# Optimization experiments

Hardware: AMD Instinct MI355X
Metric: run time of the kernel (lower is better)

Reference implementation:

```python
import jax, jax.numpy as jnp
import numpy as np

B, C, H, W = 4, 512, 64, 64
CQK = C // 8  # query/key channels


def setup_inputs() -> dict:
    key = jax.random.key(0)
    ks = jax.random.split(key, 8)
    s = 0.05
    return {
        "x": jax.random.normal(ks[0], (B, C, H, W), dtype=jnp.float32),
        "Wq": jax.random.normal(ks[1], (CQK, C), dtype=jnp.float32) * s,
        "bq": jax.random.normal(ks[2], (CQK,), dtype=jnp.float32) * s,
        "Wk": jax.random.normal(ks[3], (CQK, C), dtype=jnp.float32) * s,
        "bk": jax.random.normal(ks[4], (CQK,), dtype=jnp.float32) * s,
        "Wv": jax.random.normal(ks[5], (C, C), dtype=jnp.float32) * s,
        "bv": jax.random.normal(ks[6], (C,), dtype=jnp.float32) * s,
        "gamma": jax.random.normal(ks[7], (1,), dtype=jnp.float32),
    }


def reference(x, Wq, bq, Wk, bk, Wv, bv, gamma):
    b, c, h, w = x.shape
    hw = h * w
    # 1x1 convs == per-pixel linear projections over channels
    q = jnp.einsum('bchw,dc->bdhw', x, Wq) + bq[None, :, None, None]
    k = jnp.einsum('bchw,dc->bdhw', x, Wk) + bk[None, :, None, None]
    v = jnp.einsum('bchw,dc->bdhw', x, Wv) + bv[None, :, None, None]
    q = q.reshape(b, -1, hw)  # [B, C/8, HW]
    k = k.reshape(b, -1, hw)  # [B, C/8, HW]
    v = v.reshape(b, -1, hw)  # [B, C,   HW]
    # attn[b,i,j] = <q[:, i], k[:, j]>, softmax over j
    attn = jax.nn.softmax(jnp.einsum('bdi,bdj->bij', q, k), axis=-1)
    # out[b,c,i] = sum_j v[b,c,j] * attn[b,i,j]
    out = jnp.einsum('bcj,bij->bci', v, attn).reshape(b, c, h, w)
    return gamma[0] * out + x
```

## Files before the change

kernel.cpp:

```cpp
#include <hip/hip_runtime.h>
#include <hip/hip_bf16.h>
#include <math.h>

#define HW 4096
#define NC 512
#define NB 4

typedef float f32x4 __attribute__((ext_vector_type(4)));
typedef float f32x16 __attribute__((ext_vector_type(16)));
typedef short bf16x8 __attribute__((ext_vector_type(8)));
typedef unsigned int u32;
typedef u32 u32x4 __attribute__((ext_vector_type(4)));
typedef unsigned short ushort_t;

#define GLOAD_LDS(g, s) __builtin_amdgcn_global_load_lds((const __attribute__((address_space(1))) void*)(g), (__attribute__((address_space(3))) void*)(s), 16, 0, 0)

__device__ __forceinline__ unsigned short f2bf(float f){
  unsigned int u = __builtin_bit_cast(unsigned int, f);
  u += 0x7FFFu + ((u >> 16) & 1u);
  return (unsigned short)(u >> 16);
}
__device__ __forceinline__ float bf2f(unsigned short h){
  unsigned int u = ((unsigned int)h) << 16;
  return __builtin_bit_cast(float, u);
}

__global__ __launch_bounds__(256) void wsplit_kernel(
    const float* __restrict__ Wq, const float* __restrict__ Wk,
    const float* __restrict__ Wv, ushort_t* __restrict__ wh, ushort_t* __restrict__ wl)
{
  long e = ((long)blockIdx.x * 256 + threadIdx.x) * 8;
  int r = (int)(e >> 9), c = (int)(e & 511);
  const float* src = (r < 64)  ? Wq + (long)r * 512 + c
                   : (r < 128) ? Wk + (long)(r - 64) * 512 + c
                               : Wv + (long)(r - 128) * 512 + c;
  f32x4 v0 = *reinterpret_cast<const f32x4*>(src);
  f32x4 v1 = *reinterpret_cast<const f32x4*>(src + 4);
  ushort_t h[8], l[8];
  #pragma unroll
  for (int j = 0; j < 4; j++){ h[j] = f2bf(v0[j]); l[j] = f2bf(v0[j] - bf2f(h[j])); }
  #pragma unroll
  for (int j = 0; j < 4; j++){ h[4+j] = f2bf(v1[j]); l[4+j] = f2bf(v1[j] - bf2f(h[4+j])); }
  *reinterpret_cast<bf16x8*>(wh + e) = *reinterpret_cast<bf16x8*>(h);
  if (r < 128) *reinterpret_cast<bf16x8*>(wl + e) = *reinterpret_cast<bf16x8*>(l);
}

__global__ __launch_bounds__(256) void split_kernel(
    const float* __restrict__ x, ushort_t* __restrict__ xth, ushort_t* __restrict__ xtl)
{
  const int i0 = blockIdx.x * 64;
  const int c0 = blockIdx.y * 64;
  const int b  = blockIdx.z;
  const int tid = threadIdx.x;
  const int tx = tid & 63, ty = tid >> 6;
  __shared__ float ts[64][65];
  #pragma unroll
  for (int u = 0; u < 16; u++){
    int cl = ty * 16 + u;
    ts[cl][tx] = x[((long)b * NC + c0 + cl) * HW + i0 + tx];
  }
  __syncthreads();
  const int px = tid >> 2;
  const int cs = (tid & 3) * 16;
  ushort_t h[16], l[16];
  #pragma unroll
  for (int e = 0; e < 16; e++){
    float v = ts[cs + e][px];
    h[e] = f2bf(v);
    l[e] = f2bf(v - bf2f(h[e]));
  }
  long base = ((long)b * HW + i0 + px) * 512 + c0 + cs;
  *reinterpret_cast<bf16x8*>(xth + base)     = *reinterpret_cast<bf16x8*>(h);
  *reinterpret_cast<bf16x8*>(xth + base + 8) = *reinterpret_cast<bf16x8*>(h + 8);
  *reinterpret_cast<bf16x8*>(xtl + base)     = *reinterpret_cast<bf16x8*>(l);
  *reinterpret_cast<bf16x8*>(xtl + base + 8) = *reinterpret_cast<bf16x8*>(l + 8);
}

__global__ __launch_bounds__(256) void gemm_kernel(
    const ushort_t* __restrict__ xth, const ushort_t* __restrict__ xtl,
    const ushort_t* __restrict__ wh, const ushort_t* __restrict__ wl,
    const float* __restrict__ bq, const float* __restrict__ bk, const float* __restrict__ bv,
    ushort_t* __restrict__ qhi, ushort_t* __restrict__ qlo,
    ushort_t* __restrict__ khi, ushort_t* __restrict__ klo,
    ushort_t* __restrict__ vv)
{
  extern __shared__ char lds[];
  const int it = blockIdx.x;
  const int rg = blockIdx.y;
  const int b  = blockIdx.z;
  const int i0 = it * 128;
  const int tid = threadIdx.x;
  const int w = tid >> 6;
  const int lane = tid & 63;
  const int g = lane >> 4, n = lane & 15;
  const int wy = w >> 1, wx = w & 1;

  f32x4 acc[4][4];
  #pragma unroll
  for (int a = 0; a < 4; a++)
    #pragma unroll
    for (int m = 0; m < 4; m++) acc[a][m] = (f32x4){0.f, 0.f, 0.f, 0.f};

  const long xrow = (long)b * HW + i0;

  auto stage = [&](int bsel, int c0s){
    char* dbase = lds + bsel * 32768 + (w << 10);
    #pragma unroll
    for (int u = 0; u < 4; u++){
      int idx = (u << 8) | tid;
      int px = idx >> 3;
      int chs = (idx & 7) ^ (px & 7);
      long go = (xrow + px) * 512 + c0s + chs * 8;
      GLOAD_LDS(xth + go, dbase + (u << 12));
      GLOAD_LDS(xtl + go, dbase + 16384 + (u << 12));
    }
  };

  stage(0, 0);
  asm volatile("s_waitcnt vmcnt(0)" ::: "memory");
  __syncthreads();

  int cur = 0;
  for (int t = 0; t < 8; t++){
    const int c0 = t << 6;
    bf16x8 wfh[4][2], wfl[4][2];
    #pragma unroll
    for (int a = 0; a < 4; a++){
      long R = (long)(rg * 128 + wx * 64 + a * 16 + n) * 512 + c0 + g * 8;
      wfh[a][0] = *reinterpret_cast<const bf16x8*>(wh + R);
      wfh[a][1] = *reinterpret_cast<const bf16x8*>(wh + R + 32);
    }
    if (rg == 0){
      #pragma unroll
      for (int a = 0; a < 4; a++){
        long R = (long)(wx * 64 + a * 16 + n) * 512 + c0 + g * 8;
        wfl[a][0] = *reinterpret_cast<const bf16x8*>(wl + R);
        wfl[a][1] = *reinterpret_cast<const bf16x8*>(wl + R + 32);
      }
    }
    if (t < 7) stage(cur ^ 1, (t + 1) << 6);
    bf16x8 xh[4][2], xl[4][2];
    const char* buf = lds + cur * 32768;
    #pragma unroll
    for (int m = 0; m < 4; m++){
      int px = wy * 64 + m * 16 + n;
      const char* row = buf + px * 128;
      #pragma unroll
      for (int ks = 0; ks < 2; ks++){
        int off = (((ks << 2) | g) ^ (px & 7)) << 4;
        xh[m][ks] = *reinterpret_cast<const bf16x8*>(row + off);
        xl[m][ks] = *reinterpret_cast<const bf16x8*>(row + 16384 + off);
      }
    }
    __builtin_amdgcn_s_setprio(1);
    if (rg == 0){
      #pragma unroll
      for (int a = 0; a < 4; a++)
        #pragma unroll
        for (int m = 0; m < 4; m++)
          #pragma unroll
          for (int ks = 0; ks < 2; ks++){
            acc[a][m] = __builtin_amdgcn_mfma_f32_16x16x32_bf16(xh[m][ks], wfh[a][ks], acc[a][m], 0, 0, 0);
            acc[a][m] = __builtin_amdgcn_mfma_f32_16x16x32_bf16(xl[m][ks], wfh[a][ks], acc[a][m], 0, 0, 0);
            acc[a][m] = __builtin_amdgcn_mfma_f32_16x16x32_bf16(xh[m][ks], wfl[a][ks], acc[a][m], 0, 0, 0);
          }
    } else {
      #pragma unroll
      for (int a = 0; a < 4; a++)
        #pragma unroll
        for (int m = 0; m < 4; m++)
          #pragma unroll
          for (int ks = 0; ks < 2; ks++){
            acc[a][m] = __builtin_amdgcn_mfma_f32_16x16x32_bf16(wfh[a][ks], xh[m][ks], acc[a][m], 0, 0, 0);
            acc[a][m] = __builtin_amdgcn_mfma_f32_16x16x32_bf16(wfh[a][ks], xl[m][ks], acc[a][m], 0, 0, 0);
          }
    }
    __builtin_amdgcn_s_setprio(0);
    asm volatile("s_waitcnt vmcnt(0)" ::: "memory");
    __syncthreads();
    cur ^= 1;
  }

  if (rg == 0){
    ushort_t* hs = wx ? khi : qhi;
    ushort_t* ls = wx ? klo : qlo;
    const float* bias = wx ? bk : bq;
    const float qscale = wx ? 1.0f : 1.44269504088896f;
    #pragma unroll
    for (int a = 0; a < 4; a++){
      float bb = bias[a * 16 + n];
      #pragma unroll
      for (int m = 0; m < 4; m++){
        #pragma unroll
        for (int r4 = 0; r4 < 4; r4++){
          int px = wy * 64 + m * 16 + g * 4 + r4;
          float v = (acc[a][m][r4] + bb) * qscale;
          ushort_t h = f2bf(v);
          ushort_t l = f2bf(v - bf2f(h));
          long ad = (xrow + px) * 64 + a * 16 + n;
          hs[ad] = h;
          ls[ad] = l;
        }
      }
    }
  } else {
    #pragma unroll
    for (int a = 0; a < 4; a++){
      #pragma unroll
      for (int r4 = 0; r4 < 4; r4++){
        int C = (rg - 1) * 128 + wx * 64 + a * 16 + g * 4 + r4;
        float bb = bv[C];
        #pragma unroll
        for (int m = 0; m < 4; m++){
          int px = wy * 64 + m * 16 + n;
          vv[((long)b * NC + C) * HW + i0 + px] = f2bf(acc[a][m][r4] + bb);
        }
      }
    }
  }
}

__global__ __launch_bounds__(512, 1) void attn_kernel(
    const ushort_t* __restrict__ qhi, const ushort_t* __restrict__ qlo,
    const ushort_t* __restrict__ khi,
    const ushort_t* __restrict__ vv,
    ushort_t* __restrict__ p0, ushort_t* __restrict__ p1,
    float* __restrict__ mbuf, float* __restrict__ lbuf)
{
  extern __shared__ char smem[];
  const int wgid = blockIdx.x;
  const int xcd = wgid & 7;
  const int jh = xcd >> 2;
  const int b  = xcd & 3;
  const int qt = wgid >> 3;
  const int tid = threadIdx.x;
  const int w = tid >> 6;
  const int lane = tid & 63;
  const int q32 = lane & 31;
  const int hh = lane >> 5;
  const int rg = w >> 1, ch = w & 1;
  const int i0w = qt * 128 + rg * 32;
  const int c0w = ch * 256;
  const int jbase = jh * 2048;

  const int kj = tid >> 3;
  const int kdblk = (tid & 7) ^ (kj & 7);
  const long kgbase = ((long)b * HW + kj) * 64 + kdblk * 8;

  auto stageK = [&](int bsel, int j0){
    char* dst = smem + bsel * 8192 + (tid >> 6 << 10);
    GLOAD_LDS(khi + kgbase + (long)j0 * 64, dst);
  };
  auto stageV = [&](int bsel, int j0){
    char* dbase = smem + 16384 + bsel * 65536 + (w << 10);
    #pragma unroll
    for (int r = 0; r < 8; r++){
      int ss = (r << 9) | tid;
      int c = ss >> 3;
      int jblk = (ss & 7) ^ (c & 7);
      long goff = (long)b * (NC * HW) + (long)c * HW + j0 + jblk * 8;
      GLOAD_LDS(vv + goff, dbase + (r << 13));
    }
  };

  bf16x8 aqh[4], aql[4];
  #pragma unroll
  for (int c = 0; c < 4; c++){
    long qb = ((long)b * HW + i0w + q32) * 64 + c * 16 + hh * 8;
    aqh[c] = *reinterpret_cast<const bf16x8*>(qhi + qb);
    aql[c] = *reinterpret_cast<const bf16x8*>(qlo + qb);
  }

  f32x16 acc[8];
  #pragma unroll
  for (int ct = 0; ct < 8; ct++)
    #pragma unroll
    for (int r = 0; r < 16; r++) acc[ct][r] = 0.f;
  float mrow = -1e30f, lrow = 0.f;

  stageK(0, jbase);
  stageV(0, jbase);
  asm volatile("s_waitcnt vmcnt(0)" ::: "memory");
  __syncthreads();

  int cur = 0;
  for (int t = 0; t < 32; t++){
    if (t < 31){
      stageK(cur ^ 1, jbase + (t + 1) * 64);
      stageV(cur ^ 1, jbase + (t + 1) * 64);
    }
    f32x16 sv[2];
    {
      const char* kb0 = smem + cur * 8192;
      __builtin_amdgcn_s_setprio(1);
      #pragma unroll
      for (int jt = 0; jt < 2; jt++){
        int jrow = jt * 32 + q32;
        const char* krow = kb0 + jrow * 128;
        int r7 = jrow & 7;
        f32x16 s;
        #pragma unroll
        for (int r = 0; r < 16; r++) s[r] = 0.f;
        #pragma unroll
        for (int c = 0; c < 4; c++){
          int off = (((c << 1) | hh) ^ r7) << 4;
          bf16x8 kh = *(const bf16x8*)(krow + off);
          s = __builtin_amdgcn_mfma_f32_32x32x16_bf16(kh, aqh[c], s, 0, 0, 0);
          s = __builtin_amdgcn_mfma_f32_32x32x16_bf16(kh, aql[c], s, 0, 0, 0);
        }
        sv[jt] = s;
      }
      __builtin_amdgcn_s_setprio(0);
    }
    {
      f32x16 mx;
      #pragma unroll
      for (int r = 0; r < 16; r++) mx[r] = fmaxf(sv[0][r], sv[1][r]);
      float m8[8];
      #pragma unroll
      for (int r = 0; r < 8; r++) m8[r] = fmaxf(mx[r], mx[r + 8]);
      float m4a = fmaxf(m8[0], m8[4]), m4b = fmaxf(m8[1], m8[5]);
      float m4c = fmaxf(m8[2], m8[6]), m4d = fmaxf(m8[3], m8[7]);
      float tmx = fmaxf(fmaxf(m4a, m4b), fmaxf(m4c, m4d));
      tmx = fmaxf(tmx, __shfl_xor(tmx, 32));
      if (__any(tmx > mrow + 11.5f)){
        float mnew = fmaxf(mrow, tmx);
        float sc = exp2f(mrow - mnew);
        lrow *= sc;
        #pragma unroll
        for (int ct = 0; ct < 8; ct++)
          #pragma unroll
          for (int r = 0; r < 16; r++) acc[ct][r] *= sc;
        mrow = mnew;
      }
    }
    bf16x8 pa[4];
    {
      #pragma unroll
      for (int jt = 0; jt < 2; jt++)
        #pragma unroll
        for (int r = 0; r < 16; r++) sv[jt][r] = exp2f(sv[jt][r] - mrow);
      float rs = 0.f;
      #pragma unroll
      for (int r = 0; r < 16; r++) rs += sv[0][r] + sv[1][r];
      rs += __shfl_xor(rs, 32);
      lrow += rs;
      #pragma unroll
      for (int jt = 0; jt < 2; jt++){
        u32 pk[8];
        #pragma unroll
        for (int i = 0; i < 8; i++){
          float a = sv[jt][2 * i], bb = sv[jt][2 * i + 1];
          u32 d;
          asm("v_cvt_pk_bf16_f32 %0, %1, %2" : "=v"(d) : "v"(a), "v"(bb));
          pk[i] = d;
        }
        #pragma unroll
        for (int cc = 0; cc < 2; cc++){
          u32 a0 = pk[4 * cc + 0], b0 = pk[4 * cc + 2];
          u32 a1 = pk[4 * cc + 1], b1 = pk[4 * cc + 3];
          asm volatile("v_permlane32_swap_b32 %0, %1" : "+v"(a0), "+v"(b0));
          asm volatile("v_permlane32_swap_b32 %0, %1" : "+v"(a1), "+v"(b1));
          u32x4 wv;
          wv[0] = a0; wv[1] = a1; wv[2] = b0; wv[3] = b1;
          pa[jt * 2 + cc] = __builtin_bit_cast(bf16x8, wv);
        }
      }
    }
    {
      const char* vb = smem + 16384 + cur * 65536;
      __builtin_amdgcn_s_setprio(1);
      #pragma unroll
      for (int ct = 0; ct < 8; ct++){
        int row = c0w + ct * 32 + q32;
        const char* vrow = vb + row * 128;
        int r7 = row & 7;
        #pragma unroll
        for (int c = 0; c < 4; c++){
          int off = (((c << 1) | hh) ^ r7) << 4;
          bf16x8 vf = *(const bf16x8*)(vrow + off);
          acc[ct] = __builtin_amdgcn_mfma_f32_32x32x16_bf16(vf, pa[c], acc[ct], 0, 0, 0);
        }
      }
      __builtin_amdgcn_s_setprio(0);
    }
    asm volatile("s_waitcnt vmcnt(0)" ::: "memory");
    __syncthreads();
    cur ^= 1;
  }

  ushort_t* pd = jh ? p1 : p0;
  const int i = i0w + q32;
  #pragma unroll
  for (int ct = 0; ct < 8; ct++){
    #pragma unroll
    for (int r = 0; r < 16; r++){
      int c = c0w + ct * 32 + (r & 3) + 8 * (r >> 2) + 4 * hh;
      pd[((long)b * NC + c) * HW + i] = f2bf(acc[ct][r]);
    }
  }
  if (ch == 0 && lane < 32){
    int gi = b * HW + i0w + lane;
    mbuf[jh * (NB * HW) + gi] = mrow;
    lbuf[jh * (NB * HW) + gi] = lrow;
  }
}

__global__ __launch_bounds__(256) void comb_kernel(
    const ushort_t* __restrict__ p0, const ushort_t* __restrict__ p1,
    const float* __restrict__ mbuf, const float* __restrict__ lbuf,
    const float* __restrict__ x, const float* __restrict__ gamma,
    float* __restrict__ out)
{
  const int it = blockIdx.x;
  const int ct = blockIdx.y;
  const int b  = blockIdx.z;
  const int i0 = it * 64, c0 = ct * 64;
  const int tid = threadIdx.x;
  const int tx = tid & 63, ty = tid >> 6;
  __shared__ float f0s[64], f1s[64];
  const float gm = gamma[0];
  if (tid < 64){
    int gi = b * HW + i0 + tid;
    float m0 = mbuf[gi], m1 = mbuf[NB * HW + gi];
    float l0 = lbuf[gi], l1 = lbuf[NB * HW + gi];
    float M = fmaxf(m0, m1);
    float w0 = exp2f(m0 - M), w1 = exp2f(m1 - M);
    float rden = 1.f / (w0 * l0 + w1 * l1);
    f0s[tid] = w0 * rden;
    f1s[tid] = w1 * rden;
  }
  __syncthreads();
  #pragma unroll
  for (int u = 0; u < 16; u++){
    int cl = ty * 16 + u;
    long idx = ((long)b * NC + c0 + cl) * HW + i0 + tx;
    float o = f0s[tx] * bf2f(p0[idx]) + f1s[tx] * bf2f(p1[idx]);
    out[idx] = fmaf(gm, o, x[idx]);
  }
}

extern "C" void kernel_launch(void* const* d_in, const int* in_sizes, int n_in,
                              void* d_out, int out_size, void* d_ws, size_t ws_size,
                              hipStream_t stream)
{
  const float* x  = (const float*)d_in[0];
  const float* Wq = (const float*)d_in[1];
  const float* bq = (const float*)d_in[2];
  const float* Wk = (const float*)d_in[3];
  const float* bk = (const float*)d_in[4];
  const float* Wv = (const float*)d_in[5];
  const float* bv = (const float*)d_in[6];
  const float* gamma = (const float*)d_in[7];
  float* out = (float*)d_out;

  char* ws = (char*)d_ws;
  const size_t MB = 1024 * 1024;
  ushort_t* xth = (ushort_t*)(ws);
  ushort_t* xtl = (ushort_t*)(ws + 16 * MB);
  ushort_t* wh  = (ushort_t*)(ws + 32 * MB);
  ushort_t* wl  = (ushort_t*)(ws + 32 * MB + 655360);
  ushort_t* qhi = (ushort_t*)(ws + 33 * MB);
  ushort_t* qlo = (ushort_t*)(ws + 35 * MB);
  ushort_t* khi = (ushort_t*)(ws + 37 * MB);
  ushort_t* klo = (ushort_t*)(ws + 39 * MB);
  ushort_t* vv  = (ushort_t*)(ws + 41 * MB);
  float*    mbuf = (float*)(ws + 57 * MB);
  float*    lbuf = (float*)(ws + 57 * MB + 131072);
  ushort_t* part0 = xth;
  ushort_t* part1 = xtl;

  wsplit_kernel<<<dim3(160), dim3(256), 0, stream>>>(Wq, Wk, Wv, wh, wl);
  split_kernel<<<dim3(64, 8, NB), dim3(256), 0, stream>>>(x, xth, xtl);

  const int GSMEM = 65536;
  hipFuncSetAttribute((const void*)gemm_kernel,
                      hipFuncAttributeMaxDynamicSharedMemorySize, GSMEM);
  gemm_kernel<<<dim3(32, 5, NB), dim3(256), GSMEM, stream>>>(
      xth, xtl, wh, wl, bq, bk, bv, qhi, qlo, khi, klo, vv);

  const int ASMEM = 147456;
  hipFuncSetAttribute((const void*)attn_kernel,
                      hipFuncAttributeMaxDynamicSharedMemorySize, ASMEM);
  attn_kernel<<<dim3(256), dim3(512), ASMEM, stream>>>(
      qhi, qlo, khi, vv, part0, part1, mbuf, lbuf);

  comb_kernel<<<dim3(64, 8, NB), dim3(256), 0, stream>>>(
      part0, part1, mbuf, lbuf, x, gamma, out);
}
```

Measured before the change: 212.0 us.

## Split attention waves into producers that compute softmax and consumers that load

Before, the two waves sharing a 32-row group each recomputed the same QK scores and softmax. Now four producer waves compute S and P once and pass P, plus the per-row rescale flag and factor, to their paired consumer waves through LDS. The consumer waves issue all global-to-LDS loads for the next V and K tiles. K drops to a single buffer, LDS use grows, and an extra block barrier is added each iteration. The split leaves the producers with more work than the consumers (QK, softmax and their own PV share), which may leave the consumers idle at the barrier.

Result: faster. 198.2 us (-6.5%).

```diff
diff --git a/kernel.cpp b/kernel.cpp
--- a/kernel.cpp
+++ b/kernel.cpp
@@ -228,6 +228,7 @@
     float* __restrict__ mbuf, float* __restrict__ lbuf)
 {
   extern __shared__ char smem[];
+  const int VB = 8192, PB = 139264, FB = 155648;
   const int wgid = blockIdx.x;
   const int xcd = wgid & 7;
   const int jh = xcd >> 2;
@@ -238,65 +239,55 @@
   const int lane = tid & 63;
   const int q32 = lane & 31;
   const int hh = lane >> 5;
-  const int rg = w >> 1, ch = w & 1;
+  const bool producer = (w < 4);
+  const int rg = producer ? w : (w - 4);
+  const int ch = producer ? 0 : 1;
   const int i0w = qt * 128 + rg * 32;
   const int c0w = ch * 256;
   const int jbase = jh * 2048;
-
-  const int kj = tid >> 3;
-  const int kdblk = (tid & 7) ^ (kj & 7);
-  const long kgbase = ((long)b * HW + kj) * 64 + kdblk * 8;
-
-  auto stageK = [&](int bsel, int j0){
-    char* dst = smem + bsel * 8192 + (tid >> 6 << 10);
-    GLOAD_LDS(khi + kgbase + (long)j0 * 64, dst);
-  };
-  auto stageV = [&](int bsel, int j0){
-    char* dbase = smem + 16384 + bsel * 65536 + (w << 10);
+  const int ct256 = ((w & 3) << 6) | lane;
+
+  bf16x8 aqh[4], aql[4];
+  #pragma unroll
+  for (int c = 0; c < 4; c++){
+    long qb = ((long)b * HW + i0w + q32) * 64 + c * 16 + hh * 8;
+    aqh[c] = *reinterpret_cast<const bf16x8*>(qhi + qb);
+    aql[c] = *reinterpret_cast<const bf16x8*>(qlo + qb);
+  }
+
+  f32x16 acc[8];
+  #pragma unroll
+  for (int ct = 0; ct < 8; ct++)
+    #pragma unroll
+    for (int r = 0; r < 16; r++) acc[ct][r] = 0.f;
+  float mrow = -1e30f, lrow = 0.f;
+
+  {
+    int kj = tid >> 3;
+    int kd = (tid & 7) ^ (kj & 7);
+    GLOAD_LDS(khi + ((long)b * HW + jbase + kj) * 64 + kd * 8, smem + (w << 10));
     #pragma unroll
     for (int r = 0; r < 8; r++){
       int ss = (r << 9) | tid;
       int c = ss >> 3;
       int jblk = (ss & 7) ^ (c & 7);
-      long goff = (long)b * (NC * HW) + (long)c * HW + j0 + jblk * 8;
-      GLOAD_LDS(vv + goff, dbase + (r << 13));
-    }
-  };
-
-  bf16x8 aqh[4], aql[4];
-  #pragma unroll
-  for (int c = 0; c < 4; c++){
-    long qb = ((long)b * HW + i0w + q32) * 64 + c * 16 + hh * 8;
-    aqh[c] = *reinterpret_cast<const bf16x8*>(qhi + qb);
-    aql[c] = *reinterpret_cast<const bf16x8*>(qlo + qb);
-  }
-
-  f32x16 acc[8];
-  #pragma unroll
-  for (int ct = 0; ct < 8; ct++)
-    #pragma unroll
-    for (int r = 0; r < 16; r++) acc[ct][r] = 0.f;
-  float mrow = -1e30f, lrow = 0.f;
-
-  stageK(0, jbase);
-  stageV(0, jbase);
+      GLOAD_LDS(vv + ((long)b * NC + c) * HW + jbase + jblk * 8,
+                smem + VB + (r << 13) + (w << 10));
+    }
+  }
   asm volatile("s_waitcnt vmcnt(0)" ::: "memory");
   __syncthreads();
 
   int cur = 0;
   for (int t = 0; t < 32; t++){
-    if (t < 31){
-      stageK(cur ^ 1, jbase + (t + 1) * 64);
-      stageV(cur ^ 1, jbase + (t + 1) * 64);
-    }
-    f32x16 sv[2];
-    {
-      const char* kb0 = smem + cur * 8192;
+    bf16x8 pa[4];
+    if (producer){
+      f32x16 sv[2];
       __builtin_amdgcn_s_setprio(1);
       #pragma unroll
       for (int jt = 0; jt < 2; jt++){
         int jrow = jt * 32 + q32;
-        const char* krow = kb0 + jrow * 128;
+        const char* krow = smem + jrow * 128;
         int r7 = jrow & 7;
         f32x16 s;
         #pragma unroll
@@ -311,8 +302,6 @@
         sv[jt] = s;
       }
       __builtin_amdgcn_s_setprio(0);
-    }
-    {
       f32x16 mx;
       #pragma unroll
       for (int r = 0; r < 16; r++) mx[r] = fmaxf(sv[0][r], sv[1][r]);
@@ -323,9 +312,11 @@
       float m4c = fmaxf(m8[2], m8[6]), m4d = fmaxf(m8[3], m8[7]);
       float tmx = fmaxf(fmaxf(m4a, m4b), fmaxf(m4c, m4d));
       tmx = fmaxf(tmx, __shfl_xor(tmx, 32));
-      if (__any(tmx > mrow + 11.5f)){
+      int upd = __any(tmx > mrow + 11.5f) ? 1 : 0;
+      float sc = 1.f;
+      if (upd){
         float mnew = fmaxf(mrow, tmx);
-        float sc = exp2f(mrow - mnew);
+        sc = exp2f(mrow - mnew);
         lrow *= sc;
         #pragma unroll
         for (int ct = 0; ct < 8; ct++)
@@ -333,9 +324,6 @@
           for (int r = 0; r < 16; r++) acc[ct][r] *= sc;
         mrow = mnew;
       }
-    }
-    bf16x8 pa[4];
-    {
       #pragma unroll
       for (int jt = 0; jt < 2; jt++)
         #pragma unroll
@@ -366,9 +354,53 @@
           pa[jt * 2 + cc] = __builtin_bit_cast(bf16x8, wv);
         }
       }
+      char* pb = smem + PB + rg * 4096 + lane * 64;
+      #pragma unroll
+      for (int i = 0; i < 4; i++)
+        *reinterpret_cast<bf16x8*>(pb + ((i ^ (lane & 3)) << 4)) = pa[i];
+      if (lane == 0) *(int*)(smem + FB + rg * 4) = upd;
+      if (upd && hh == 0) *(float*)(smem + FB + 64 + rg * 128 + q32 * 4) = sc;
+    } else {
+      if (t < 31){
+        char* dbase = smem + VB + ((cur ^ 1) << 16) + ((w & 3) << 10);
+        int j0 = jbase + (t + 1) * 64;
+        #pragma unroll
+        for (int r = 0; r < 16; r++){
+          int ss = (r << 8) | ct256;
+          int c = ss >> 3;
+          int jblk = (ss & 7) ^ (c & 7);
+          GLOAD_LDS(vv + ((long)b * NC + c) * HW + j0 + jblk * 8, dbase + (r << 12));
+        }
+      }
+    }
+    __syncthreads();
+    if (!producer){
+      if (t < 31){
+        int j0 = jbase + (t + 1) * 64;
+        #pragma unroll
+        for (int r = 0; r < 2; r++){
+          int chunk = (r << 8) | ct256;
+          int kj = chunk >> 3;
+          int kd = (chunk & 7) ^ (kj & 7);
+          GLOAD_LDS(khi + ((long)b * HW + j0 + kj) * 64 + kd * 8,
+                    smem + (r << 12) + ((w & 3) << 10));
+        }
+      }
+      const char* pb = smem + PB + rg * 4096 + lane * 64;
+      #pragma unroll
+      for (int i = 0; i < 4; i++)
+        pa[i] = *reinterpret_cast<const bf16x8*>(pb + ((i ^ (lane & 3)) << 4));
+      int updf = *(const int*)(smem + FB + rg * 4);
+      if (updf){
+        float sc = *(const float*)(smem + FB + 64 + rg * 128 + q32 * 4);
+        #pragma unroll
+        for (int ct = 0; ct < 8; ct++)
+          #pragma unroll
+          for (int r = 0; r < 16; r++) acc[ct][r] *= sc;
+      }
     }
     {
-      const char* vb = smem + 16384 + cur * 65536;
+      const char* vb = smem + VB + (cur << 16);
       __builtin_amdgcn_s_setprio(1);
       #pragma unroll
       for (int ct = 0; ct < 8; ct++){
@@ -399,7 +431,7 @@
       pd[((long)b * NC + c) * HW + i] = f2bf(acc[ct][r]);
     }
   }
-  if (ch == 0 && lane < 32){
+  if (producer && lane < 32){
     int gi = b * HW + i0w + lane;
     mbuf[jh * (NB * HW) + gi] = mrow;
     lbuf[jh * (NB * HW) + gi] = lrow;
@@ -479,7 +511,7 @@
   gemm_kernel<<<dim3(32, 5, NB), dim3(256), GSMEM, stream>>>(
       xth, xtl, wh, wl, bq, bk, bv, qhi, qlo, khi, klo, vv);
 
-  const int ASMEM = 147456;
+  const int ASMEM = 156672;
   hipFuncSetAttribute((const void*)attn_kernel,
                       hipFuncAttributeMaxDynamicSharedMemorySize, ASMEM);
   attn_kernel<<<dim3(256), dim3(512), ASMEM, stream>>>(
```

## Software-pipeline attention loop with 32-key tiles and triple-buffered V

Applied to the files above, without the earlier changes.

Restructures the attention main loop to work on 32-key tiles instead of 64. V is triple-buffered and K double-buffered, with loads issued two tiles ahead, and the QK^T plus softmax for the next tile is computed after the current PV MFMAs. This lets softmax overlap with outstanding loads and MFMA work. The wait now drains only partially (vmcnt(4)) before the barrier instead of fully, and LDS use drops. In exchange there are twice as many barriers and iterations, and the hi/lo QK products go into separate accumulators that are summed afterwards.

After: 218.8 us. 3.2% more time.

```diff
diff --git a/kernel.cpp b/kernel.cpp
--- a/kernel.cpp
+++ b/kernel.cpp
@@ -228,6 +228,7 @@
     float* __restrict__ mbuf, float* __restrict__ lbuf)
 {
   extern __shared__ char smem[];
+  const int KB = 98304;
   const int wgid = blockIdx.x;
   const int xcd = wgid & 7;
   const int jh = xcd >> 2;
@@ -243,26 +244,6 @@
   const int c0w = ch * 256;
   const int jbase = jh * 2048;
 
-  const int kj = tid >> 3;
-  const int kdblk = (tid & 7) ^ (kj & 7);
-  const long kgbase = ((long)b * HW + kj) * 64 + kdblk * 8;
-
-  auto stageK = [&](int bsel, int j0){
-    char* dst = smem + bsel * 8192 + (tid >> 6 << 10);
-    GLOAD_LDS(khi + kgbase + (long)j0 * 64, dst);
-  };
-  auto stageV = [&](int bsel, int j0){
-    char* dbase = smem + 16384 + bsel * 65536 + (w << 10);
-    #pragma unroll
-    for (int r = 0; r < 8; r++){
-      int ss = (r << 9) | tid;
-      int c = ss >> 3;
-      int jblk = (ss & 7) ^ (c & 7);
-      long goff = (long)b * (NC * HW) + (long)c * HW + j0 + jblk * 8;
-      GLOAD_LDS(vv + goff, dbase + (r << 13));
-    }
-  };
-
   bf16x8 aqh[4], aql[4];
   #pragma unroll
   for (int c = 0; c < 4; c++){
@@ -277,116 +258,140 @@
     #pragma unroll
     for (int r = 0; r < 16; r++) acc[ct][r] = 0.f;
   float mrow = -1e30f, lrow = 0.f;
+  bf16x8 pa[2];
+
+  auto stageV = [&](int vbsel, int j0){
+    char* vd = smem + vbsel * 32768;
+    #pragma unroll
+    for (int u = 0; u < 4; u++){
+      int ci = (w << 8) | (u << 6) | lane;
+      int R = ci >> 3, half = (ci >> 2) & 1, pos = ci & 3;
+      int jc = pos ^ (R & 3);
+      int c = 2 * R + half;
+      GLOAD_LDS(vv + ((long)b * NC + c) * HW + j0 + jc * 8, vd + ci * 16);
+    }
+  };
+  auto stageK = [&](int kbsel, int j0){
+    if (lane < 32){
+      int ci = (w << 5) | lane;
+      int kj = ci >> 3, pos = ci & 7;
+      int db = pos ^ (kj & 7);
+      GLOAD_LDS(khi + ((long)b * HW + j0 + kj) * 64 + db * 8,
+                smem + KB + (kbsel << 12) + ci * 16);
+    }
+  };
+
+  auto qk_sm = [&](int tt){
+    const char* krow = smem + KB + ((tt & 1) << 12) + q32 * 128;
+    const int r7 = q32 & 7;
+    f32x16 s1, s2;
+    #pragma unroll
+    for (int r = 0; r < 16; r++){ s1[r] = 0.f; s2[r] = 0.f; }
+    __builtin_amdgcn_s_setprio(1);
+    #pragma unroll
+    for (int c = 0; c < 4; c++){
+      int off = (((c << 1) | hh) ^ r7) << 4;
+      bf16x8 kh = *(const bf16x8*)(krow + off);
+      s1 = __builtin_amdgcn_mfma_f32_32x32x16_bf16(kh, aqh[c], s1, 0, 0, 0);
+      s2 = __builtin_amdgcn_mfma_f32_32x32x16_bf16(kh, aql[c], s2, 0, 0, 0);
+    }
+    __builtin_amdgcn_s_setprio(0);
+    f32x16 sv;
+    #pragma unroll
+    for (int r = 0; r < 16; r++) sv[r] = s1[r] + s2[r];
+    float m8[8];
+    #pragma unroll
+    for (int r = 0; r < 8; r++) m8[r] = fmaxf(sv[r], sv[r + 8]);
+    float m4a = fmaxf(m8[0], m8[4]), m4b = fmaxf(m8[1], m8[5]);
+    float m4c = fmaxf(m8[2], m8[6]), m4d = fmaxf(m8[3], m8[7]);
+    float tmx = fmaxf(fmaxf(m4a, m4b), fmaxf(m4c, m4d));
+    tmx = fmaxf(tmx, __shfl_xor(tmx, 32));
+    if (__any(tmx > mrow + 11.5f)){
+      float mnew = fmaxf(mrow, tmx);
+      float sc = exp2f(mrow - mnew);
+      lrow *= sc;
+      #pragma unroll
+      for (int ct = 0; ct < 8; ct++)
+        #pragma unroll
+        for (int r = 0; r < 16; r++) acc[ct][r] *= sc;
+      mrow = mnew;
+    }
+    #pragma unroll
+    for (int r = 0; r < 16; r++) sv[r] = exp2f(sv[r] - mrow);
+    float rs = 0.f;
+    #pragma unroll
+    for (int r = 0; r < 16; r++) rs += sv[r];
+    rs += __shfl_xor(rs, 32);
+    lrow += rs;
+    u32 pk[8];
+    #pragma unroll
+    for (int i = 0; i < 8; i++){
+      float a = sv[2 * i], bb = sv[2 * i + 1];
+      u32 d;
+      asm("v_cvt_pk_bf16_f32 %0, %1, %2" : "=v"(d) : "v"(a), "v"(bb));
+      pk[i] = d;
+    }
+    #pragma unroll
+    for (int cc = 0; cc < 2; cc++){
+      u32 a0 = pk[4 * cc + 0], b0 = pk[4 * cc + 2];
+      u32 a1 = pk[4 * cc + 1], b1 = pk[4 * cc + 3];
+      asm volatile("v_permlane32_swap_b32 %0, %1" : "+v"(a0), "+v"(b0));
+      asm volatile("v_permlane32_swap_b32 %0, %1" : "+v"(a1), "+v"(b1));
+      u32x4 wv;
+      wv[0] = a0; wv[1] = a1; wv[2] = b0; wv[3] = b1;
+      pa[cc] = __builtin_bit_cast(bf16x8, wv);
+    }
+  };
 
   stageK(0, jbase);
+  stageK(1, jbase + 32);
   stageV(0, jbase);
+  stageV(1, jbase + 32);
   asm volatile("s_waitcnt vmcnt(0)" ::: "memory");
-  __syncthreads();
-
-  int cur = 0;
-  for (int t = 0; t < 32; t++){
-    if (t < 31){
-      stageK(cur ^ 1, jbase + (t + 1) * 64);
-      stageV(cur ^ 1, jbase + (t + 1) * 64);
-    }
-    f32x16 sv[2];
+  __builtin_amdgcn_s_barrier();
+  __builtin_amdgcn_sched_barrier(0);
+
+  qk_sm(0);
+  __builtin_amdgcn_sched_barrier(0);
+  __builtin_amdgcn_s_barrier();
+  __builtin_amdgcn_sched_barrier(0);
+
+  for (int t = 0; t < 64; t++){
+    if (t < 62){
+      int j2 = jbase + (t + 2) * 32;
+      stageK(t & 1, j2);
+      stageV((t + 2) % 3, j2);
+    }
     {
-      const char* kb0 = smem + cur * 8192;
+      const char* vb = smem + (t % 3) * 32768;
       __builtin_amdgcn_s_setprio(1);
       #pragma unroll
-      for (int jt = 0; jt < 2; jt++){
-        int jrow = jt * 32 + q32;
-        const char* krow = kb0 + jrow * 128;
-        int r7 = jrow & 7;
-        f32x16 s;
-        #pragma unroll
-        for (int r = 0; r < 16; r++) s[r] = 0.f;
-        #pragma unroll
-        for (int c = 0; c < 4; c++){
-          int off = (((c << 1) | hh) ^ r7) << 4;
-          bf16x8 kh = *(const bf16x8*)(krow + off);
-          s = __builtin_amdgcn_mfma_f32_32x32x16_bf16(kh, aqh[c], s, 0, 0, 0);
-          s = __builtin_amdgcn_mfma_f32_32x32x16_bf16(kh, aql[c], s, 0, 0, 0);
-        }
-        sv[jt] = s;
-      }
-      __builtin_amdgcn_s_setprio(0);
-    }
-    {
-      f32x16 mx;
-      #pragma unroll
-      for (int r = 0; r < 16; r++) mx[r] = fmaxf(sv[0][r], sv[1][r]);
-      float m8[8];
-      #pragma unroll
-      for (int r = 0; r < 8; r++) m8[r] = fmaxf(mx[r], mx[r + 8]);
-      float m4a = fmaxf(m8[0], m8[4]), m4b = fmaxf(m8[1], m8[5]);
-      float m4c = fmaxf(m8[2], m8[6]), m4d = fmaxf(m8[3], m8[7]);
-      float tmx = fmaxf(fmaxf(m4a, m4b), fmaxf(m4c, m4d));
-      tmx = fmaxf(tmx, __shfl_xor(tmx, 32));
-      if (__any(tmx > mrow + 11.5f)){
-        float mnew = fmaxf(mrow, tmx);
-        float sc = exp2f(mrow - mnew);
-        lrow *= sc;
-        #pragma unroll
-        for (int ct = 0; ct < 8; ct++)
-          #pragma unroll
-          for (int r = 0; r < 16; r++) acc[ct][r] *= sc;
-        mrow = mnew;
-      }
-    }
-    bf16x8 pa[4];
-    {
-      #pragma unroll
-      for (int jt = 0; jt < 2; jt++)
-        #pragma unroll
-        for (int r = 0; r < 16; r++) sv[jt][r] = exp2f(sv[jt][r] - mrow);
-      float rs = 0.f;
-      #pragma unroll
-      for (int r = 0; r < 16; r++) rs += sv[0][r] + sv[1][r];
-      rs += __shfl_xor(rs, 32);
-      lrow += rs;
-      #pragma unroll
-      for (int jt = 0; jt < 2; jt++){
-        u32 pk[8];
-        #pragma unroll
-        for (int i = 0; i < 8; i++){
-          float a = sv[jt][2 * i], bb = sv[jt][2 * i + 1];
-          u32 d;
-          asm("v_cvt_pk_bf16_f32 %0, %1, %2" : "=v"(d) : "v"(a), "v"(bb));
-          pk[i] = d;
-        }
-        #pragma unroll
-        for (int cc = 0; cc < 2; cc++){
-          u32 a0 = pk[4 * cc + 0], b0 = pk[4 * cc + 2];
-          u32 a1 = pk[4 * cc + 1], b1 = pk[4 * cc + 3];
-          asm volatile("v_permlane32_swap_b32 %0, %1" : "+v"(a0), "+v"(b0));
-          asm volatile("v_permlane32_swap_b32 %0, %1" : "+v"(a1), "+v"(b1));
-          u32x4 wv;
-          wv[0] = a0; wv[1] = a1; wv[2] = b0; wv[3] = b1;
-          pa[jt * 2 + cc] = __builtin_bit_cast(bf16x8, wv);
-        }
-      }
-    }
-    {
-      const char* vb = smem + 16384 + cur * 65536;
-      __builtin_amdgcn_s_setprio(1);
-      #pragma unroll
       for (int ct = 0; ct < 8; ct++){
-        int row = c0w + ct * 32 + q32;
-        const char* vrow = vb + row * 128;
-        int r7 = row & 7;
-        #pragma unroll
-        for (int c = 0; c < 4; c++){
-          int off = (((c << 1) | hh) ^ r7) << 4;
-          bf16x8 vf = *(const bf16x8*)(vrow + off);
-          acc[ct] = __builtin_amdgcn_mfma_f32_32x32x16_bf16(vf, pa[c], acc[ct], 0, 0, 0);
+        int c = c0w + ct * 32 + q32;
+        int R = c >> 1;
+        const char* vrow = vb + R * 128 + (c & 1) * 64;
+        int r3 = R & 3;
+        #pragma unroll
+        for (int ks = 0; ks < 2; ks++){
+          int pos = ((ks << 1) | hh) ^ r3;
+          bf16x8 vf = *(const bf16x8*)(vrow + pos * 16);
+          acc[ct] = __builtin_amdgcn_mfma_f32_32x32x16_bf16(vf, pa[ks], acc[ct], 0, 0, 0);
         }
       }
       __builtin_amdgcn_s_setprio(0);
     }
-    asm volatile("s_waitcnt vmcnt(0)" ::: "memory");
-    __syncthreads();
-    cur ^= 1;
+    if (t < 63) qk_sm(t + 1);
+    if (t < 62){
+      __builtin_amdgcn_sched_barrier(0);
+      asm volatile("s_waitcnt vmcnt(4)" ::: "memory");
+      __builtin_amdgcn_s_barrier();
+      __builtin_amdgcn_sched_barrier(0);
+    } else if (t == 62){
+      __builtin_amdgcn_sched_barrier(0);
+      asm volatile("s_waitcnt vmcnt(0)" ::: "memory");
+      __builtin_amdgcn_s_barrier();
+      __builtin_amdgcn_sched_barrier(0);
+    }
   }
 
   ushort_t* pd = jh ? p1 : p0;
@@ -479,7 +484,7 @@
   gemm_kernel<<<dim3(32, 5, NB), dim3(256), GSMEM, stream>>>(
       xth, xtl, wh, wl, bq, bk, bv, qhi, qlo, khi, klo, vv);
 
-  const int ASMEM = 147456;
+  const int ASMEM = 106496;
   hipFuncSetAttribute((const void*)attn_kernel,
                       hipFuncAttributeMaxDynamicSharedMemorySize, ASMEM);
   attn_kernel<<<dim3(256), dim3(512), ASMEM, stream>>>(
```

## Split QK^T across wave pairs and exchange P tiles via LDS

Applied to the files above, without the earlier changes.

Previously each of the two waves sharing a row group computed the full 64-column score tile redundantly. Now each wave computes its own 32-column half, writes its packed P fragment and its row max to LDS, and after a barrier reads the partner's half to form the full PV operand. Max rescaling is deferred by one iteration using the previous step's combined max, and each half keeps its own running sum, which the combine kernel now adds. K staging becomes single-buffered and is issued after the barrier, the trailing vmcnt wait is removed, and an extra barrier plus more LDS are added per iteration.

Measured after the change: 496.3 us. +134.1%, slower.

```diff
diff --git a/kernel.cpp b/kernel.cpp
--- a/kernel.cpp
+++ b/kernel.cpp
@@ -228,6 +228,7 @@
     float* __restrict__ mbuf, float* __restrict__ lbuf)
 {
   extern __shared__ char smem[];
+  const int VB = 8192, PA = 139264, TM = 155648;
   const int wgid = blockIdx.x;
   const int xcd = wgid & 7;
   const int jh = xcd >> 2;
@@ -243,132 +244,137 @@
   const int c0w = ch * 256;
   const int jbase = jh * 2048;
 
-  const int kj = tid >> 3;
-  const int kdblk = (tid & 7) ^ (kj & 7);
-  const long kgbase = ((long)b * HW + kj) * 64 + kdblk * 8;
-
-  auto stageK = [&](int bsel, int j0){
-    char* dst = smem + bsel * 8192 + (tid >> 6 << 10);
-    GLOAD_LDS(khi + kgbase + (long)j0 * 64, dst);
+  bf16x8 aqh[4], aql[4];
+  #pragma unroll
+  for (int c = 0; c < 4; c++){
+    long qb = ((long)b * HW + i0w + q32) * 64 + c * 16 + hh * 8;
+    aqh[c] = *reinterpret_cast<const bf16x8*>(qhi + qb);
+    aql[c] = *reinterpret_cast<const bf16x8*>(qlo + qb);
+  }
+
+  f32x16 acc[8];
+  #pragma unroll
+  for (int ct = 0; ct < 8; ct++)
+    #pragma unroll
+    for (int r = 0; r < 16; r++) acc[ct][r] = 0.f;
+  float mrow = 0.f, lrow = 0.f, tmx_prev = -1e30f;
+
+  auto stageK = [&](int j0){
+    int ci = (w << 6) | lane;
+    int kj = ci >> 3, pos = ci & 7;
+    int db = pos ^ (kj & 7);
+    GLOAD_LDS(khi + ((long)b * HW + j0 + kj) * 64 + db * 8, smem + (w << 10));
   };
-  auto stageV = [&](int bsel, int j0){
-    char* dbase = smem + 16384 + bsel * 65536 + (w << 10);
+  auto stageV = [&](int vbsel, int j0){
+    char* dbase = smem + VB + (vbsel << 16) + (w << 10);
     #pragma unroll
     for (int r = 0; r < 8; r++){
       int ss = (r << 9) | tid;
       int c = ss >> 3;
       int jblk = (ss & 7) ^ (c & 7);
-      long goff = (long)b * (NC * HW) + (long)c * HW + j0 + jblk * 8;
-      GLOAD_LDS(vv + goff, dbase + (r << 13));
+      GLOAD_LDS(vv + ((long)b * NC + c) * HW + j0 + jblk * 8, dbase + (r << 13));
     }
   };
 
-  bf16x8 aqh[4], aql[4];
-  #pragma unroll
-  for (int c = 0; c < 4; c++){
-    long qb = ((long)b * HW + i0w + q32) * 64 + c * 16 + hh * 8;
-    aqh[c] = *reinterpret_cast<const bf16x8*>(qhi + qb);
-    aql[c] = *reinterpret_cast<const bf16x8*>(qlo + qb);
-  }
-
-  f32x16 acc[8];
-  #pragma unroll
-  for (int ct = 0; ct < 8; ct++)
-    #pragma unroll
-    for (int r = 0; r < 16; r++) acc[ct][r] = 0.f;
-  float mrow = -1e30f, lrow = 0.f;
-
-  stageK(0, jbase);
+  stageK(jbase);
   stageV(0, jbase);
   asm volatile("s_waitcnt vmcnt(0)" ::: "memory");
   __syncthreads();
 
   int cur = 0;
   for (int t = 0; t < 32; t++){
-    if (t < 31){
-      stageK(cur ^ 1, jbase + (t + 1) * 64);
-      stageV(cur ^ 1, jbase + (t + 1) * 64);
-    }
-    f32x16 sv[2];
+    if (t > 0){
+      float ptmx = *(const float*)(smem + TM + (((t - 1) & 1) << 10) + ((w ^ 1) << 7) + (q32 << 2));
+      float cand = fmaxf(tmx_prev, ptmx);
+      if (__any(cand > mrow + 11.5f)){
+        float mnew = fmaxf(mrow, cand);
+        float sc = exp2f(mrow - mnew);
+        lrow *= sc;
+        #pragma unroll
+        for (int ct = 0; ct < 8; ct++)
+          #pragma unroll
+          for (int r = 0; r < 16; r++) acc[ct][r] *= sc;
+        mrow = mnew;
+      }
+    }
+    f32x16 sv;
     {
-      const char* kb0 = smem + cur * 8192;
+      int jrow = ch * 32 + q32;
+      const char* krow = smem + jrow * 128;
+      int r7 = jrow & 7;
+      f32x16 s1, s2;
+      #pragma unroll
+      for (int r = 0; r < 16; r++){ s1[r] = 0.f; s2[r] = 0.f; }
       __builtin_amdgcn_s_setprio(1);
       #pragma unroll
-      for (int jt = 0; jt < 2; jt++){
-        int jrow = jt * 32 + q32;
-        const char* krow = kb0 + jrow * 128;
-        int r7 = jrow & 7;
-        f32x16 s;
-        #pragma unroll
-        for (int r = 0; r < 16; r++) s[r] = 0.f;
-        #pragma unroll
-        for (int c = 0; c < 4; c++){
-          int off = (((c << 1) | hh) ^ r7) << 4;
-          bf16x8 kh = *(const bf16x8*)(krow + off);
-          s = __builtin_amdgcn_mfma_f32_32x32x16_bf16(kh, aqh[c], s, 0, 0, 0);
-          s = __builtin_amdgcn_mfma_f32_32x32x16_bf16(kh, aql[c], s, 0, 0, 0);
-        }
-        sv[jt] = s;
+      for (int c = 0; c < 4; c++){
+        int off = (((c << 1) | hh) ^ r7) << 4;
+        bf16x8 kh = *(const bf16x8*)(krow + off);
+        s1 = __builtin_amdgcn_mfma_f32_32x32x16_bf16(kh, aqh[c], s1, 0, 0, 0);
+        s2 = __builtin_amdgcn_mfma_f32_32x32x16_bf16(kh, aql[c], s2, 0, 0, 0);
       }
       __builtin_amdgcn_s_setprio(0);
+      #pragma unroll
+      for (int r = 0; r < 16; r++) sv[r] = s1[r] + s2[r];
     }
     {
-      f32x16 mx;
-      #pragma unroll
-      for (int r = 0; r < 16; r++) mx[r] = fmaxf(sv[0][r], sv[1][r]);
       float m8[8];
       #pragma unroll
-      for (int r = 0; r < 8; r++) m8[r] = fmaxf(mx[r], mx[r + 8]);
+      for (int r = 0; r < 8; r++) m8[r] = fmaxf(sv[r], sv[r + 8]);
       float m4a = fmaxf(m8[0], m8[4]), m4b = fmaxf(m8[1], m8[5]);
       float m4c = fmaxf(m8[2], m8[6]), m4d = fmaxf(m8[3], m8[7]);
       float tmx = fmaxf(fmaxf(m4a, m4b), fmaxf(m4c, m4d));
       tmx = fmaxf(tmx, __shfl_xor(tmx, 32));
-      if (__any(tmx > mrow + 11.5f)){
-        float mnew = fmaxf(mrow, tmx);
-        float sc = exp2f(mrow - mnew);
-        lrow *= sc;
-        #pragma unroll
-        for (int ct = 0; ct < 8; ct++)
-          #pragma unroll
-          for (int r = 0; r < 16; r++) acc[ct][r] *= sc;
-        mrow = mnew;
-      }
-    }
-    bf16x8 pa[4];
+      if (hh == 0)
+        *(float*)(smem + TM + ((t & 1) << 10) + (w << 7) + (q32 << 2)) = tmx;
+      tmx_prev = tmx;
+    }
+    bf16x8 own0, own1;
     {
       #pragma unroll
-      for (int jt = 0; jt < 2; jt++)
-        #pragma unroll
-        for (int r = 0; r < 16; r++) sv[jt][r] = exp2f(sv[jt][r] - mrow);
+      for (int r = 0; r < 16; r++) sv[r] = exp2f(sv[r] - mrow);
       float rs = 0.f;
       #pragma unroll
-      for (int r = 0; r < 16; r++) rs += sv[0][r] + sv[1][r];
+      for (int r = 0; r < 16; r++) rs += sv[r];
       rs += __shfl_xor(rs, 32);
       lrow += rs;
-      #pragma unroll
-      for (int jt = 0; jt < 2; jt++){
-        u32 pk[8];
-        #pragma unroll
-        for (int i = 0; i < 8; i++){
-          float a = sv[jt][2 * i], bb = sv[jt][2 * i + 1];
-          u32 d;
-          asm("v_cvt_pk_bf16_f32 %0, %1, %2" : "=v"(d) : "v"(a), "v"(bb));
-          pk[i] = d;
-        }
-        #pragma unroll
-        for (int cc = 0; cc < 2; cc++){
-          u32 a0 = pk[4 * cc + 0], b0 = pk[4 * cc + 2];
-          u32 a1 = pk[4 * cc + 1], b1 = pk[4 * cc + 3];
-          asm volatile("v_permlane32_swap_b32 %0, %1" : "+v"(a0), "+v"(b0));
-          asm volatile("v_permlane32_swap_b32 %0, %1" : "+v"(a1), "+v"(b1));
-          u32x4 wv;
-          wv[0] = a0; wv[1] = a1; wv[2] = b0; wv[3] = b1;
-          pa[jt * 2 + cc] = __builtin_bit_cast(bf16x8, wv);
-        }
-      }
-    }
+      u32 pk[8];
+      #pragma unroll
+      for (int i = 0; i < 8; i++){
+        float a = sv[2 * i], bb = sv[2 * i + 1];
+        u32 d;
+        asm("v_cvt_pk_bf16_f32 %0, %1, %2" : "=v"(d) : "v"(a), "v"(bb));
+        pk[i] = d;
+      }
+      u32 a0 = pk[0], b0 = pk[2], a1 = pk[1], b1 = pk[3];
+      asm volatile("v_permlane32_swap_b32 %0, %1" : "+v"(a0), "+v"(b0));
+      asm volatile("v_permlane32_swap_b32 %0, %1" : "+v"(a1), "+v"(b1));
+      u32x4 wv0; wv0[0] = a0; wv0[1] = a1; wv0[2] = b0; wv0[3] = b1;
+      own0 = __builtin_bit_cast(bf16x8, wv0);
+      u32 a2 = pk[4], b2 = pk[6], a3 = pk[5], b3 = pk[7];
+      asm volatile("v_permlane32_swap_b32 %0, %1" : "+v"(a2), "+v"(b2));
+      asm volatile("v_permlane32_swap_b32 %0, %1" : "+v"(a3), "+v"(b3));
+      u32x4 wv1; wv1[0] = a2; wv1[1] = a3; wv1[2] = b2; wv1[3] = b3;
+      own1 = __builtin_bit_cast(bf16x8, wv1);
+      char* pb = smem + PA + (w << 11);
+      *reinterpret_cast<bf16x8*>(pb + (lane << 4)) = own0;
+      *reinterpret_cast<bf16x8*>(pb + 1024 + (lane << 4)) = own1;
+    }
+    __syncthreads();
+    bf16x8 pa4[4];
     {
-      const char* vb = smem + 16384 + cur * 65536;
+      pa4[ch * 2 + 0] = own0;
+      pa4[ch * 2 + 1] = own1;
+      const char* qb2 = smem + PA + ((w ^ 1) << 11);
+      pa4[(1 - ch) * 2 + 0] = *reinterpret_cast<const bf16x8*>(qb2 + (lane << 4));
+      pa4[(1 - ch) * 2 + 1] = *reinterpret_cast<const bf16x8*>(qb2 + 1024 + (lane << 4));
+    }
+    if (t < 31){
+      stageK(jbase + (t + 1) * 64);
+      stageV(cur ^ 1, jbase + (t + 1) * 64);
+    }
+    {
+      const char* vb = smem + VB + (cur << 16);
       __builtin_amdgcn_s_setprio(1);
       #pragma unroll
       for (int ct = 0; ct < 8; ct++){
@@ -379,12 +385,11 @@
         for (int c = 0; c < 4; c++){
           int off = (((c << 1) | hh) ^ r7) << 4;
           bf16x8 vf = *(const bf16x8*)(vrow + off);
-          acc[ct] = __builtin_amdgcn_mfma_f32_32x32x16_bf16(vf, pa[c], acc[ct], 0, 0, 0);
+          acc[ct] = __builtin_amdgcn_mfma_f32_32x32x16_bf16(vf, pa4[c], acc[ct], 0, 0, 0);
         }
       }
       __builtin_amdgcn_s_setprio(0);
     }
-    asm volatile("s_waitcnt vmcnt(0)" ::: "memory");
     __syncthreads();
     cur ^= 1;
   }
@@ -399,10 +404,10 @@
       pd[((long)b * NC + c) * HW + i] = f2bf(acc[ct][r]);
     }
   }
-  if (ch == 0 && lane < 32){
+  if (lane < 32){
     int gi = b * HW + i0w + lane;
-    mbuf[jh * (NB * HW) + gi] = mrow;
-    lbuf[jh * (NB * HW) + gi] = lrow;
+    if (ch == 0) mbuf[jh * (NB * HW) + gi] = mrow;
+    lbuf[(jh * 2 + ch) * (NB * HW) + gi] = lrow;
   }
 }
 
@@ -412,6 +417,7 @@
     const float* __restrict__ x, const float* __restrict__ gamma,
     float* __restrict__ out)
 {
+  const int NBHW = NB * HW;
   const int it = blockIdx.x;
   const int ct = blockIdx.y;
   const int b  = blockIdx.z;
@@ -422,8 +428,9 @@
   const float gm = gamma[0];
   if (tid < 64){
     int gi = b * HW + i0 + tid;
-    float m0 = mbuf[gi], m1 = mbuf[NB * HW + gi];
-    float l0 = lbuf[gi], l1 = lbuf[NB * HW + gi];
+    float m0 = mbuf[gi], m1 = mbuf[NBHW + gi];
+    float l0 = lbuf[gi] + lbuf[NBHW + gi];
+    float l1 = lbuf[2 * NBHW + gi] + lbuf[3 * NBHW + gi];
     float M = fmaxf(m0, m1);
     float w0 = exp2f(m0 - M), w1 = exp2f(m1 - M);
     float rden = 1.f / (w0 * l0 + w1 * l1);
@@ -479,7 +486,7 @@
   gemm_kernel<<<dim3(32, 5, NB), dim3(256), GSMEM, stream>>>(
       xth, xtl, wh, wl, bq, bk, bv, qhi, qlo, khi, klo, vv);
 
-  const int ASMEM = 147456;
+  const int ASMEM = 157696;
   hipFuncSetAttribute((const void*)attn_kernel,
                       hipFuncAttributeMaxDynamicSharedMemorySize, ASMEM);
   attn_kernel<<<dim3(256), dim3(512), ASMEM, stream>>>(
```
